# Performance work log

Hardware: AMD Instinct MI355X
Metric: run time of the kernel (lower is better)

## Reference

```python
import jax, jax.numpy as jnp
import numpy as np

# Production GravNet config: 8 events x 4096 hits, K=40 neighbours, 4 spatial dims
B, V, K, S, P, F_IN, F_OUT = 8, 4096, 40, 4, 64, 64, 128
N = B * V
MAX_RADIUS_SQ = 1.0  # SelectKnn(max_radius=1.0)


def setup_inputs() -> dict:
    key = jax.random.key(0)
    ks = jax.random.split(key, 7)
    x = jax.random.normal(ks[0], (N, F_IN), jnp.float32)
    # Dense layer params (glorot-ish scaling)
    W_prop = jax.random.normal(ks[1], (F_IN, P), jnp.float32) / np.sqrt(F_IN)
    b_prop = jnp.zeros((P,), jnp.float32)
    W_sp = jax.random.normal(ks[2], (F_IN, S), jnp.float32) / np.sqrt(F_IN)
    b_sp = jnp.zeros((S,), jnp.float32)
    # output transform input dim = n_prop_total (2*P) + F_IN
    W_out = jax.random.normal(ks[3], (2 * P + F_IN, F_OUT), jnp.float32) / np.sqrt(2 * P + F_IN)
    b_out = jnp.zeros((F_OUT,), jnp.float32)
    row_splits = jnp.arange(B + 1, dtype=jnp.int32) * V  # equal-size ragged segments
    return dict(x=x, W_prop=W_prop, b_prop=b_prop, W_sp=W_sp, b_sp=b_sp,
                W_out=W_out, b_out=b_out, row_splits=row_splits)


def _knn_indices(coords):
    """Per-event brute-force KNN. coords: [N,S] -> global neighbour idx [N,K]."""
    c = coords.reshape(B, V, S)
    # pairwise squared distances within each event: [B,V,V]
    d = jnp.sum((c[:, :, None, :] - c[:, None, :, :]) ** 2, axis=-1)
    neg_d, idx = jax.lax.top_k(-d, K + 1)  # nearest first; col 0 is self (d=0)
    idx, dsq = idx[:, :, 1:], -neg_d[:, :, 1:]
    # tf_compatible max_radius: out-of-radius neighbours -> self index
    self_idx = jnp.arange(V, dtype=idx.dtype)[None, :, None]
    idx = jnp.where(dsq > MAX_RADIUS_SQ, self_idx, idx)
    gidx = idx + (jnp.arange(B, dtype=idx.dtype) * V)[:, None, None]
    return gidx.reshape(N, K)


def reference(x, W_prop, b_prop, W_sp, b_sp, W_out, b_out, row_splits):
    coords = x @ W_sp + b_sp                      # [N,S] learned coordinates
    nidx = _knn_indices(coords)                   # [N,K] (int, non-diff)
    nb_coords = coords[nidx]                      # [N,K,S] gather
    dsq = jnp.sum((coords[:, None, :] - nb_coords) ** 2, axis=-1)  # [N,K]
    feat = x @ W_prop + b_prop                    # [N,P]
    w = jnp.exp(-10.0 * dsq)[:, :, None]          # gauss_of_lin(10*d^2)
    nf = feat[nidx] * w                           # [N,K,P]
    agg = jnp.concatenate([nf.max(axis=1), nf.mean(axis=1)], axis=-1)  # [N,2P]
    out = jnp.tanh(jnp.concatenate([agg, x], axis=-1) @ W_out + b_out)  # [N,F_OUT]
    return out
```

## Files before the change

### kernel.cpp

```cpp
#include <hip/hip_runtime.h>
#include <cstdint>
#include <cstddef>

#define NB   8
#define VV   4096
#define KNN  40
#define NTOT 32768
#define CAP  256
#define INFB 0x7F800000u
#define ONEB 0x3F800000u

__global__ __launch_bounds__(256) void k_prep(
    const float* __restrict__ x, const float* __restrict__ W_prop,
    const float* __restrict__ b_prop, const float* __restrict__ W_sp,
    const float* __restrict__ b_sp, const float* __restrict__ W_out,
    float* __restrict__ coords, float* __restrict__ feat,
    float* __restrict__ xW)
{
  __shared__ float xt[64][64];
  const int t = threadIdx.x;
  const int row0 = blockIdx.x * 64;

  #pragma unroll
  for (int i = 0; i < 16; ++i) {
    int idx = t + i * 256;
    xt[idx >> 6][idx & 63] = x[(size_t)row0 * 64 + idx];
  }
  __syncthreads();

  {
    const int col = t & 63, rb = (t >> 6) * 16;
    float acc[16];
    #pragma unroll
    for (int i = 0; i < 16; ++i) acc[i] = b_prop[col];
    for (int k = 0; k < 64; k += 4) {
      const float w0 = W_prop[(k + 0) * 64 + col];
      const float w1 = W_prop[(k + 1) * 64 + col];
      const float w2 = W_prop[(k + 2) * 64 + col];
      const float w3 = W_prop[(k + 3) * 64 + col];
      #pragma unroll
      for (int i = 0; i < 16; ++i) {
        const float4 a4 = *(const float4*)&xt[rb + i][k];
        acc[i] += a4.x * w0 + a4.y * w1 + a4.z * w2 + a4.w * w3;
      }
    }
    #pragma unroll
    for (int i = 0; i < 16; ++i)
      feat[(size_t)(row0 + rb + i) * 64 + col] = acc[i];
  }

  {
    const int col = t & 127, who = t >> 7;
    #pragma unroll
    for (int p = 0; p < 2; ++p) {
      const int rb = who * 16 + p * 32;
      float acc[16];
      #pragma unroll
      for (int i = 0; i < 16; ++i) acc[i] = 0.f;
      for (int k = 0; k < 64; k += 4) {
        const float w0 = W_out[(size_t)(128 + k + 0) * 128 + col];
        const float w1 = W_out[(size_t)(128 + k + 1) * 128 + col];
        const float w2 = W_out[(size_t)(128 + k + 2) * 128 + col];
        const float w3 = W_out[(size_t)(128 + k + 3) * 128 + col];
        #pragma unroll
        for (int i = 0; i < 16; ++i) {
          const float4 a4 = *(const float4*)&xt[rb + i][k];
          acc[i] += a4.x * w0 + a4.y * w1 + a4.z * w2 + a4.w * w3;
        }
      }
      #pragma unroll
      for (int i = 0; i < 16; ++i)
        xW[(size_t)(row0 + rb + i) * 128 + col] = acc[i];
    }
  }

  if (t < 64) {
    float a0 = b_sp[0], a1 = b_sp[1], a2 = b_sp[2], a3 = b_sp[3];
    for (int k = 0; k < 64; ++k) {
      const float xv = xt[t][k];
      a0 += xv * W_sp[k * 4 + 0];
      a1 += xv * W_sp[k * 4 + 1];
      a2 += xv * W_sp[k * 4 + 2];
      a3 += xv * W_sp[k * 4 + 3];
    }
    ((float4*)coords)[row0 + t] = make_float4(a0, a1, a2, a3);
  }
}

template <int NC>
__device__ __forceinline__ unsigned bs40(const uint2* __restrict__ list,
                                         int M, int lane) {
  unsigned dv[NC];
  #pragma unroll
  for (int j = 0; j < NC; ++j) {
    const int e = lane + j * 64;
    dv[j] = (e < M) ? list[e].x : INFB;
  }
  unsigned lo = 0, hi = ONEB;
  while (lo < hi) {
    const unsigned mid = (lo + hi) >> 1;
    int cnt = 0;
    #pragma unroll
    for (int j = 0; j < NC; ++j)
      cnt += (int)__popcll(__ballot(dv[j] <= mid));
    if (cnt >= KNN) hi = mid; else lo = mid + 1;
  }
  return hi;
}

#define AGG_CHUNK(J0, N)                                                     \
  {                                                                          \
    float fv[N], wgt[N];                                                     \
    _Pragma("unroll")                                                        \
    for (int j = 0; j < N; ++j) {                                            \
      const uint2 en = list[(J0) + j];              \
      wgt[j] = __expf(-10.f * __uint_as_float(en.x));                        \
      const int ei = __builtin_amdgcn_readfirstlane((int)en.y);              \
      fv[j] = fe[(size_t)ei * 64 + lane];        \
    }                                                                        \
    _Pragma("unroll")                                                        \
    for (int j = 0; j < N; ++j) {                                            \
      const float v = fv[j] * wgt[j];                                        \
      vmax = fmaxf(vmax, v);                                                 \
      vsum += v;                                                             \
    }                                                                        \
  }

__global__ __launch_bounds__(512, 4) void k_knn(
    const float* __restrict__ coords, const float* __restrict__ feat,
    float* __restrict__ agg)
{
  __shared__ float4 cs[VV];
  __shared__ uint2 lists[8][CAP];

  const int t = threadIdx.x, lane = t & 63;
  const int wvid = __builtin_amdgcn_readfirstlane(t) >> 6;
  const int bid0 = blockIdx.x;
  const int bid = (bid0 & 7) * 64 + (bid0 >> 3);
  const int ev = bid >> 6;
  const int qbase = (bid & 63) * 64;
  const int evbase = ev * VV;

  {
    const float4* cg = (const float4*)coords + evbase;
    for (int i = t; i < VV; i += 512) cs[i] = cg[i];
  }
  __syncthreads();

  uint2* list = lists[wvid];
  const float* fe = feat + (size_t)evbase * 64;
  const unsigned long long lmask = (1ull << lane) - 1ull;

  auto scan = [&](unsigned rbits, int q, float4 qc) -> int {
    int M = 0;
    #pragma unroll 4
    for (int base = 0; base < VV; base += 64) {
      const int c = base + lane;
      const float4 cc = cs[c];
      const float dx = qc.x - cc.x, dy = qc.y - cc.y;
      const float dz = qc.z - cc.z, dw = qc.w - cc.w;
      const float dsq = dx * dx + dy * dy + dz * dz + dw * dw;
      const bool pred = (__float_as_uint(dsq) <= rbits) && (c != q);
      const unsigned long long bm = __ballot(pred);
      if (pred) {
        const int pos = M + (int)__popcll(bm & lmask);
        if (pos < CAP)
          list[pos] = make_uint2(__float_as_uint(dsq), (unsigned)c);
      }
      M += (int)__popcll(bm);
    }
    return M;
  };

  for (int qi = 0; qi < 8; ++qi) {
    const int q = qbase + wvid * 8 + qi;
    const float4 qc = cs[q];

    int M = scan(ONEB, q, qc);
    bool ok = true;

    if (M > CAP) {
      const unsigned t0 = bs40<4>(list, CAP, lane);
      M = scan(t0, q, qc);
      ok = (M <= CAP);
    }

    float vmax = -__builtin_inff(), vsum = 0.f;

    if (ok) {
      int Msel;
      if (M > KNN) {
        unsigned taub;
        if      (M <=  64) taub = bs40<1>(list, M, lane);
        else if (M <= 128) taub = bs40<2>(list, M, lane);
        else               taub = bs40<4>(list, M, lane);
        int S = 0;
        for (int be = 0; be < M; be += 64) {
          const int e = be + lane;
          uint2 en = make_uint2(0u, 0u);
          bool p = false;
          if (e < M) { en = list[e]; p = (en.x <= taub); }
          const unsigned long long bm = __ballot(p);
          if (p) list[S + (int)__popcll(bm & lmask)] = en;
          S += (int)__popcll(bm);
        }
        Msel = S;
      } else {
        if (lane >= M && lane < KNN)
          list[lane] = make_uint2(0u, (unsigned)q);
        Msel = KNN;
      }

      if (Msel == KNN) {
        AGG_CHUNK(0, 16)
        AGG_CHUNK(16, 16)
        AGG_CHUNK(32, 8)
      } else {
        #pragma unroll 4
        for (int e = 0; e < Msel; ++e) {
          const uint2 en = list[e];
          const int ei = __builtin_amdgcn_readfirstlane((int)en.y);
          const float w = __expf(-10.f * __uint_as_float(en.x));
          const float v = fe[(size_t)ei * 64 + lane] * w;
          vmax = fmaxf(vmax, v);
          vsum += v;
        }
      }
    } else {
      unsigned lo = 0, hi = ONEB;
      while (lo < hi) {
        const unsigned mid = (lo + hi) >> 1;
        const float fm = __uint_as_float(mid);
        int cnt = 0;
        for (int base = 0; base < VV; base += 64) {
          const int c = base + lane;
          const float4 cc = cs[c];
          const float dx = qc.x - cc.x, dy = qc.y - cc.y;
          const float dz = qc.z - cc.z, dw = qc.w - cc.w;
          const float dsq = dx * dx + dy * dy + dz * dz + dw * dw;
          cnt += (int)__popcll(__ballot(dsq <= fm && c != q));
        }
        if (cnt >= KNN) hi = mid; else lo = mid + 1;
      }
      const float tau = __uint_as_float(hi);
      for (int c = 0; c < VV; ++c) {
        if (c == q) continue;
        const float4 cc = cs[c];
        const float dx = qc.x - cc.x, dy = qc.y - cc.y;
        const float dz = qc.z - cc.z, dw = qc.w - cc.w;
        const float dsq = dx * dx + dy * dy + dz * dz + dw * dw;
        if (dsq <= tau) {
          const float w = __expf(-10.f * dsq);
          const float v = fe[(size_t)c * 64 + lane] * w;
          vmax = fmaxf(vmax, v);
          vsum += v;
        }
      }
    }

    const int g = evbase + q;
    agg[(size_t)g * 128 + lane]      = vmax;
    agg[(size_t)g * 128 + 64 + lane] = vsum * (1.f / 40.f);
  }
}

__global__ __launch_bounds__(256) void k_out(
    const float* __restrict__ agg, const float* __restrict__ W_out,
    const float* __restrict__ b_out, float* __restrict__ out)
{
  __shared__ float at[64][128];
  const int t = threadIdx.x;
  const int row0 = blockIdx.x * 64;

  #pragma unroll
  for (int i = 0; i < 32; ++i) {
    int idx = t + i * 256;
    at[idx >> 7][idx & 127] = agg[(size_t)row0 * 128 + idx];
  }
  __syncthreads();

  const int col = t & 127, who = t >> 7;
  #pragma unroll
  for (int p = 0; p < 2; ++p) {
    const int rb = who * 16 + p * 32;
    float acc[16];
    #pragma unroll
    for (int i = 0; i < 16; ++i) acc[i] = 0.f;
    for (int k = 0; k < 128; k += 4) {
      const float w0 = W_out[(size_t)(k + 0) * 128 + col];
      const float w1 = W_out[(size_t)(k + 1) * 128 + col];
      const float w2 = W_out[(size_t)(k + 2) * 128 + col];
      const float w3 = W_out[(size_t)(k + 3) * 128 + col];
      #pragma unroll
      for (int i = 0; i < 16; ++i) {
        const float4 a4 = *(const float4*)&at[rb + i][k];
        acc[i] += a4.x * w0 + a4.y * w1 + a4.z * w2 + a4.w * w3;
      }
    }
    const float bb = b_out[col];
    #pragma unroll
    for (int i = 0; i < 16; ++i) {
      const size_t o = (size_t)(row0 + rb + i) * 128 + col;
      float v = acc[i] + bb + out[o];
      v = fminf(15.f, fmaxf(-15.f, v));
      const float e = __expf(2.f * v);
      out[o] = (e - 1.f) / (e + 1.f);
    }
  }
}

extern "C" void kernel_launch(void* const* d_in, const int* in_sizes, int n_in,
                              void* d_out, int out_size, void* d_ws, size_t ws_size,
                              hipStream_t stream) {
  const float* x      = (const float*)d_in[0];
  const float* W_prop = (const float*)d_in[1];
  const float* b_prop = (const float*)d_in[2];
  const float* W_sp   = (const float*)d_in[3];
  const float* b_sp   = (const float*)d_in[4];
  const float* W_out  = (const float*)d_in[5];
  const float* b_out  = (const float*)d_in[6];

  float* out = (float*)d_out;
  char* ws = (char*)d_ws;
  float* coords = (float*)ws;
  float* feat   = (float*)(ws + (512 << 10));
  float* agg    = (float*)(ws + (512 << 10) + (8 << 20));

  k_prep<<<NTOT / 64, 256, 0, stream>>>(x, W_prop, b_prop, W_sp, b_sp, W_out,
                                        coords, feat, out );
  k_knn<<<NB * (VV / 64), 512, 0, stream>>>(coords, feat, agg);
  k_out<<<NTOT / 64, 256, 0, stream>>>(agg, W_out, b_out, out);
}
```

Baseline: 206.2 us.

## Bucket-sort coordinates by x and restrict KNN scan to radius window

A new per-event kernel sorts the learned coordinates into 256 buckets along the first axis and records a permutation plus bucket prefix offsets. The KNN kernel then scans only the candidates whose x-bucket lies within the max radius of the query, instead of all 4096 points. Neighbour indices are mapped back through the permutation before the features are gathered, and results are written to the original row. The list capacity is also reduced, which lowers LDS use. The cost is an extra launch with only eight blocks, plus indirection loads, and the fallback path now searches only within the window.

```diff
diff --git a/kernel.cpp b/kernel.cpp
--- a/kernel.cpp
+++ b/kernel.cpp
@@ -6,9 +6,14 @@
 #define VV   4096
 #define KNN  40
 #define NTOT 32768
-#define CAP  256
+#define CAP  224
 #define INFB 0x7F800000u
 #define ONEB 0x3F800000u
+
+__device__ __forceinline__ int xbucket(float x) {
+  int b = (int)floorf((x + 4.f) * 32.f);
+  return b < 0 ? 0 : (b > 255 ? 255 : b);
+}
 
 __global__ __launch_bounds__(256) void k_prep(
     const float* __restrict__ x, const float* __restrict__ W_prop,
@@ -87,6 +92,55 @@
   }
 }
 
+__global__ __launch_bounds__(512) void k_sort(
+    float* __restrict__ coords, unsigned short* __restrict__ perm,
+    unsigned short* __restrict__ prefg)
+{
+  __shared__ float4 cs[VV];
+  __shared__ int hist[256];
+  __shared__ int pref[257];
+  const int t = threadIdx.x, ev = blockIdx.x;
+  const int evbase = ev * VV;
+  float4* cg = (float4*)coords + evbase;
+
+  for (int i = t; i < VV; i += 512) cs[i] = cg[i];
+  if (t < 256) hist[t] = 0;
+  __syncthreads();
+
+  for (int i = t; i < VV; i += 512)
+    atomicAdd(&hist[xbucket(cs[i].x)], 1);
+  __syncthreads();
+
+  if (t < 64) {
+    const int l = t;
+    const int h0 = hist[4*l], h1 = hist[4*l+1], h2 = hist[4*l+2], h3 = hist[4*l+3];
+    const int s = h0 + h1 + h2 + h3;
+    int incl = s;
+    #pragma unroll
+    for (int off = 1; off < 64; off <<= 1) {
+      const int v = __shfl_up(incl, off);
+      if (l >= off) incl += v;
+    }
+    const int excl = incl - s;
+    pref[4*l]   = excl;
+    pref[4*l+1] = excl + h0;
+    pref[4*l+2] = excl + h0 + h1;
+    pref[4*l+3] = excl + h0 + h1 + h2;
+    if (l == 63) pref[256] = excl + s;
+  }
+  __syncthreads();
+  if (t < 256) hist[t] = 0;
+  __syncthreads();
+
+  for (int i = t; i < VV; i += 512) {
+    const int b = xbucket(cs[i].x);
+    const int pos = pref[b] + atomicAdd(&hist[b], 1);
+    cg[pos] = cs[i];
+    perm[evbase + pos] = (unsigned short)i;
+  }
+  if (t < 257) prefg[ev * 257 + t] = (unsigned short)pref[t];
+}
+
 template <int NC>
 __device__ __forceinline__ unsigned bs40(const uint2* __restrict__ list,
                                          int M, int lane) {
@@ -113,10 +167,10 @@
     float fv[N], wgt[N];                                                     \
     _Pragma("unroll")                                                        \
     for (int j = 0; j < N; ++j) {                                            \
-      const uint2 en = list[(J0) + j];              \
+      const uint2 en = list[(J0) + j];                                       \
       wgt[j] = __expf(-10.f * __uint_as_float(en.x));                        \
       const int ei = __builtin_amdgcn_readfirstlane((int)en.y);              \
-      fv[j] = fe[(size_t)ei * 64 + lane];        \
+      fv[j] = fe[(size_t)ei * 64 + lane];                                    \
     }                                                                        \
     _Pragma("unroll")                                                        \
     for (int j = 0; j < N; ++j) {                                            \
@@ -127,23 +181,27 @@
   }
 
 __global__ __launch_bounds__(512, 4) void k_knn(
-    const float* __restrict__ coords, const float* __restrict__ feat,
-    float* __restrict__ agg)
+    const float* __restrict__ coords,
+    const unsigned short* __restrict__ perm,
+    const unsigned short* __restrict__ prefg,
+    const float* __restrict__ feat, float* __restrict__ agg)
 {
   __shared__ float4 cs[VV];
   __shared__ uint2 lists[8][CAP];
+  __shared__ unsigned short pr[257];
 
   const int t = threadIdx.x, lane = t & 63;
   const int wvid = __builtin_amdgcn_readfirstlane(t) >> 6;
   const int bid0 = blockIdx.x;
   const int bid = (bid0 & 7) * 64 + (bid0 >> 3);
   const int ev = bid >> 6;
-  const int qbase = (bid & 63) * 64;
+  const int slot = bid & 63;
   const int evbase = ev * VV;
 
   {
     const float4* cg = (const float4*)coords + evbase;
     for (int i = t; i < VV; i += 512) cs[i] = cg[i];
+    if (t < 257) pr[t] = prefg[ev * 257 + t];
   }
   __syncthreads();
 
@@ -151,16 +209,20 @@
   const float* fe = feat + (size_t)evbase * 64;
   const unsigned long long lmask = (1ull << lane) - 1ull;
 
-  auto scan = [&](unsigned rbits, int q, float4 qc) -> int {
+  auto scan = [&](unsigned rbits, int q, float4 qc, int lo, int hi) -> int {
     int M = 0;
-    #pragma unroll 4
-    for (int base = 0; base < VV; base += 64) {
+    #pragma unroll 2
+    for (int base = lo; base < hi; base += 64) {
       const int c = base + lane;
-      const float4 cc = cs[c];
-      const float dx = qc.x - cc.x, dy = qc.y - cc.y;
-      const float dz = qc.z - cc.z, dw = qc.w - cc.w;
-      const float dsq = dx * dx + dy * dy + dz * dz + dw * dw;
-      const bool pred = (__float_as_uint(dsq) <= rbits) && (c != q);
+      bool pred = false;
+      float dsq = 0.f;
+      if (c < hi) {
+        const float4 cc = cs[c];
+        const float dx = qc.x - cc.x, dy = qc.y - cc.y;
+        const float dz = qc.z - cc.z, dw = qc.w - cc.w;
+        dsq = dx * dx + dy * dy + dz * dz + dw * dw;
+        pred = (__float_as_uint(dsq) <= rbits) && (c != q);
+      }
       const unsigned long long bm = __ballot(pred);
       if (pred) {
         const int pos = M + (int)__popcll(bm & lmask);
@@ -173,21 +235,34 @@
   };
 
   for (int qi = 0; qi < 8; ++qi) {
-    const int q = qbase + wvid * 8 + qi;
+    const int q = slot + (wvid * 8 + qi) * 64;
     const float4 qc = cs[q];
-
-    int M = scan(ONEB, q, qc);
+    const int origq = (int)perm[evbase + q];
+    const int bq = xbucket(qc.x);
+    const int wlo = pr[bq > 32 ? bq - 32 : 0];
+    const int whi = pr[bq + 33 > 256 ? 256 : bq + 33];
+
+    int M = scan(ONEB, q, qc, wlo, whi);
     bool ok = true;
 
     if (M > CAP) {
       const unsigned t0 = bs40<4>(list, CAP, lane);
-      M = scan(t0, q, qc);
+      M = scan(t0, q, qc, wlo, whi);
       ok = (M <= CAP);
     }
 
     float vmax = -__builtin_inff(), vsum = 0.f;
 
     if (ok) {
+      for (int be = 0; be < M; be += 64) {
+        const int e = be + lane;
+        if (e < M) {
+          uint2 en = list[e];
+          en.y = (unsigned)perm[evbase + (int)en.y];
+          list[e] = en;
+        }
+      }
+
       int Msel;
       if (M > KNN) {
         unsigned taub;
@@ -207,7 +282,7 @@
         Msel = S;
       } else {
         if (lane >= M && lane < KNN)
-          list[lane] = make_uint2(0u, (unsigned)q);
+          list[lane] = make_uint2(0u, (unsigned)origq);
         Msel = KNN;
       }
 
@@ -232,33 +307,38 @@
         const unsigned mid = (lo + hi) >> 1;
         const float fm = __uint_as_float(mid);
         int cnt = 0;
-        for (int base = 0; base < VV; base += 64) {
+        for (int base = wlo; base < whi; base += 64) {
           const int c = base + lane;
-          const float4 cc = cs[c];
-          const float dx = qc.x - cc.x, dy = qc.y - cc.y;
-          const float dz = qc.z - cc.z, dw = qc.w - cc.w;
-          const float dsq = dx * dx + dy * dy + dz * dz + dw * dw;
-          cnt += (int)__popcll(__ballot(dsq <= fm && c != q));
+          bool p = false;
+          if (c < whi) {
+            const float4 cc = cs[c];
+            const float dx = qc.x - cc.x, dy = qc.y - cc.y;
+            const float dz = qc.z - cc.z, dw = qc.w - cc.w;
+            const float dsq = dx * dx + dy * dy + dz * dz + dw * dw;
+            p = (dsq <= fm && c != q);
+          }
+          cnt += (int)__popcll(__ballot(p));
         }
         if (cnt >= KNN) hi = mid; else lo = mid + 1;
       }
       const float tau = __uint_as_float(hi);
-      for (int c = 0; c < VV; ++c) {
+      for (int c = wlo; c < whi; ++c) {
         if (c == q) continue;
         const float4 cc = cs[c];
         const float dx = qc.x - cc.x, dy = qc.y - cc.y;
         const float dz = qc.z - cc.z, dw = qc.w - cc.w;
         const float dsq = dx * dx + dy * dy + dz * dz + dw * dw;
         if (dsq <= tau) {
+          const int ei = (int)perm[evbase + c];
           const float w = __expf(-10.f * dsq);
-          const float v = fe[(size_t)c * 64 + lane] * w;
+          const float v = fe[(size_t)ei * 64 + lane] * w;
           vmax = fmaxf(vmax, v);
           vsum += v;
         }
       }
     }
 
-    const int g = evbase + q;
+    const int g = evbase + origq;
     agg[(size_t)g * 128 + lane]      = vmax;
     agg[(size_t)g * 128 + 64 + lane] = vsum * (1.f / 40.f);
   }
@@ -322,12 +402,15 @@
 
   float* out = (float*)d_out;
   char* ws = (char*)d_ws;
-  float* coords = (float*)ws;
-  float* feat   = (float*)(ws + (512 << 10));
-  float* agg    = (float*)(ws + (512 << 10) + (8 << 20));
+  float* coords          = (float*)ws;
+  float* feat            = (float*)(ws + (512 << 10));
+  float* agg             = (float*)(ws + (512 << 10) + (8 << 20));
+  unsigned short* perm   = (unsigned short*)(ws + (512 << 10) + (24 << 20));
+  unsigned short* prefg  = (unsigned short*)(ws + (512 << 10) + (24 << 20) + (64 << 10));
 
   k_prep<<<NTOT / 64, 256, 0, stream>>>(x, W_prop, b_prop, W_sp, b_sp, W_out,
                                         coords, feat, out );
-  k_knn<<<NB * (VV / 64), 512, 0, stream>>>(coords, feat, agg);
+  k_sort<<<NB, 512, 0, stream>>>(coords, perm, prefg);
+  k_knn<<<NB * (VV / 64), 512, 0, stream>>>(coords, perm, prefg, feat, agg);
   k_out<<<NTOT / 64, 256, 0, stream>>>(agg, W_out, b_out, out);
 }
```

Result: slower. 211.9 us (+2.8%).
